# Optimization experiments

Measured on AMD Instinct MI355X. Metric: run time of the kernel, lower is better.

## Reference

```python
import jax, jax.numpy as jnp
from jax import lax
import numpy as np


def tridiagonal_solve(K, f):
    """Batched Thomas-algorithm solve of A(K) u = f.

    K: [..., m] diffusion coefficient at m grid points.
    f: broadcastable to [..., m-1] right-hand side.
    Returns u: [..., m-1].
    """
    n = K.shape[-1] - 1  # number of unknowns
    h2 = 1.0 / (n * n)
    f = jnp.broadcast_to(f, (*K.shape[:-1], n))

    denom0 = 2.0 * K[..., 0] + K[..., 1]
    c0 = -K[..., 1] / denom0  # [...]
    u0 = f[..., 0] / denom0

    # Forward elimination sweep, j = 1 .. n-2, as a scan over the grid axis.
    Kj = jnp.moveaxis(K[..., 1:n - 1], -1, 0)   # [n-2, ...] = K[..., j]
    Kj1 = jnp.moveaxis(K[..., 2:n], -1, 0)      # [n-2, ...] = K[..., j+1]
    fj = jnp.moveaxis(f[..., 1:n - 1], -1, 0)   # [n-2, ...]

    def fwd_step(carry, x):
        c_prev, u_prev = carry
        kj, kj1, fv = x
        denom = kj + kj1 + kj * c_prev
        c = -kj1 / denom
        u = (fv + kj * u_prev) / denom
        return (c, u), (c, u)

    _, (cs, us) = lax.scan(fwd_step, (c0, u0), (Kj, Kj1, fj))
    c_all = jnp.concatenate([c0[None], cs], axis=0)  # [n-1, ...] indices 0..n-2
    u_all = jnp.concatenate([u0[None], us], axis=0)  # [n-1, ...]

    Kn1 = K[..., n - 1]
    u_last = (f[..., n - 1] + Kn1 * u_all[-1]) / (Kn1 + Kn1 * c_all[-1])  # u[n-1]

    # Back substitution: u[j] -= c[j] * u[j+1], j = n-2 .. 0 (reverse scan).
    def bwd_step(u_next, x):
        cj, uj = x
        u_new = uj - cj * u_next
        return u_new, u_new

    _, u_head = lax.scan(bwd_step, u_last, (c_all, u_all), reverse=True)  # [n-1, ...]
    u_full = jnp.concatenate([u_head, u_last[None]], axis=0)  # [n, ...]
    return h2 * jnp.moveaxis(u_full, 0, -1)


def setup_inputs() -> dict:
    key = jax.random.key(0)
    k1, k2 = jax.random.split(key)
    B, M = 16384, 1024  # batch, grid points (n = M - 1 unknowns)
    alpha = jax.random.normal(k1, (B, M), dtype=jnp.float32)
    f_rhs = jax.random.normal(k2, (M - 1,), dtype=jnp.float32)
    return {"alpha": alpha, "f_rhs": f_rhs}


def reference(alpha, f_rhs):
    # DiffusionModel1d.forward: u = A(exp(alpha))^{-1} f_rhs
    return tridiagonal_solve(jnp.exp(alpha), f_rhs)
```

## Files before the change

### kernel.cpp

```cpp
#include <hip/hip_runtime.h>
#include <math.h>


constexpr int BT   = 16384;
constexpr int MPTS = 1024;
constexpr int NU   = 1023;
constexpr int CS   = 16;
constexpr int WPB  = 8;

__device__ __forceinline__ float frcp(float x) {
    float r = __builtin_amdgcn_rcpf(x);
    r = fmaf(r, fmaf(-x, r, 1.0f), r);
    return r;
}
__device__ __forceinline__ double drcp(double x) {
    double r = __builtin_amdgcn_rcp(x);
    r = fma(r, fma(-x, r, 1.0), r);
    return r;
}
__device__ __forceinline__ int sw(int j) { return j + (j >> 5); }

__global__ __launch_bounds__(WPB * 64, 6)
void pt_kernel(const float* __restrict__ alpha,
               const float* __restrict__ f_rhs,
               float* __restrict__ out) {
    const int t    = threadIdx.x;
    const int lane = t & 63;
    const int w    = t >> 6;
    const int row  = blockIdx.x * WPB + w;
    const int s    = lane * CS;

    __shared__ float f_lds[1056];
    __shared__ float ostage[WPB][1056];

    const float h2 = (float)(1.0 / (1023.0 * 1023.0));
    for (int i = t; i < NU; i += WPB * 64) f_lds[sw(i)] = h2 * f_rhs[i];
    if (t == 0) f_lds[sw(1023)] = 0.0f;

    const float* arow = alpha + (size_t)row * MPTS;
    float kf[CS + 1];
    #pragma unroll
    for (int q = 0; q < 4; ++q) {
        const float4 v = *reinterpret_cast<const float4*>(arow + s + 4 * q);
        kf[4 * q + 0] = expf(v.x);
        kf[4 * q + 1] = expf(v.y);
        kf[4 * q + 2] = expf(v.z);
        kf[4 * q + 3] = expf(v.w);
    }
    {
        float kx = (lane < 63) ? arow[s + CS] : 0.0f;
        kf[CS] = expf(kx);
    }
    if (lane == 63) kf[15] = 0.0f;

    __syncthreads();

    float cA[CS], uA[CS], vA[CS];
    {
        float cp = (lane == 0) ? 1.0f : 0.0f;
        float up = 0.0f, vp = 1.0f;
        #pragma unroll
        for (int i = 0; i < CS; ++i) {
            const int j = s + i;
            const float kc = kf[i];
            const float kn = kf[i + 1];
            const float b  = kc + kn;
            const float f  = f_lds[sw(j)];
            const float den = fmaf(kc, cp, b);
            const float r   = frcp(den);
            float ci = -kn * r;
            const float ui = fmaf(kc, up, f) * r;
            const float vi = (kc * vp) * r;
            if (i == CS - 1) ci = (lane == 63) ? 0.0f : ci;
            cA[i] = ci; uA[i] = ui; vA[i] = vi;
            cp = ci; up = ui; vp = vi;
        }
    }

    float De_f, Ae_f, Be_f, Ds_f, As_f, Bs_f;
    {
        float Dn = uA[CS - 1], An = vA[CS - 1], Bn = -cA[CS - 1];
        De_f = Dn; Ae_f = An; Be_f = Bn;
        uA[CS - 1] = Dn; vA[CS - 1] = An; cA[CS - 1] = Bn;
        #pragma unroll
        for (int i = CS - 2; i >= 0; --i) {
            const float ci = cA[i];
            Dn = fmaf(-ci, Dn, uA[i]);
            An = fmaf(-ci, An, vA[i]);
            Bn = -ci * Bn;
            uA[i] = Dn; vA[i] = An; cA[i] = Bn;
        }
        Ds_f = uA[0]; As_f = vA[0]; Bs_f = cA[0];
    }

    const double Ds = (double)Ds_f, As = (double)As_f, Bs = (double)Bs_f;
    const double De = (double)De_f, Ae = (double)Ae_f, Be = (double)Be_f;
    double m00 = Bs;
    double m01 = fma(Bs, De, -(Ds * Be));
    double m02 = Ds;
    double m11 = fma(Bs, Ae, -(As * Be));
    double m12 = As;
    double m21 = -Be;

    #pragma unroll
    for (int dlt = 1; dlt < 64; dlt <<= 1) {
        const bool val = (lane + dlt) < 64;
        double b00 = __shfl_down(m00, dlt); b00 = val ? b00 : 1.0;
        double b01 = __shfl_down(m01, dlt); b01 = val ? b01 : 0.0;
        double b02 = __shfl_down(m02, dlt); b02 = val ? b02 : 0.0;
        double b11 = __shfl_down(m11, dlt); b11 = val ? b11 : 1.0;
        double b12 = __shfl_down(m12, dlt); b12 = val ? b12 : 0.0;
        double b21 = __shfl_down(m21, dlt); b21 = val ? b21 : 0.0;
        const double n00 = m00 * b00;
        const double n01 = fma(m00, b01, fma(m01, b11, m02 * b21));
        const double n02 = fma(m00, b02, fma(m01, b12, m02));
        const double n11 = fma(m11, b11, m12 * b21);
        const double n12 = fma(m11, b12, m12);
        const double n21 = fma(m21, b11, b21);
        const double n22 = fma(m21, b12, 1.0);
        const double rn = drcp(n22);
        m00 = n00 * rn; m01 = n01 * rn; m02 = n02 * rn;
        m11 = n11 * rn; m12 = n12 * rn; m21 = n21 * rn;
    }
    const double alf = m02;
    const double bet = m12;
    double alfn = __shfl_down(alf, 1); alfn = (lane == 63) ? 0.0 : alfn;
    double betn = __shfl_down(bet, 1); betn = (lane == 63) ? 0.0 : betn;

    const double tt = drcp(fma(-Be, betn, 1.0));
    const double dl = fma(Be, alfn, De) * tt;
    const double gm = Ae * tt;

    double X = dl, G = gm;
    #pragma unroll
    for (int dlt = 1; dlt < 64; dlt <<= 1) {
        double bx = __shfl_up(X, dlt);
        double bg = __shfl_up(G, dlt);
        const bool val = lane >= dlt;
        bx = val ? bx : 0.0;
        bg = val ? bg : 1.0;
        X = fma(G, bx, X);
        G = G * bg;
    }
    double xp = __shfl_up(X, 1);
    const double uLd = (lane == 0) ? 0.0 : xp;
    const double Y   = fma(bet, uLd, alf);
    double yn = __shfl_down(Y, 1);
    const double uRd = (lane == 63) ? 0.0 : yn;

    const float uL = (float)uLd;
    const float uR = (float)uRd;
    float* ost = ostage[w];
    #pragma unroll
    for (int i = 0; i < CS; ++i) {
        const float uu = fmaf(vA[i], uL, fmaf(cA[i], uR, uA[i]));
        ost[sw(s + i)] = uu;
    }
    asm volatile("s_waitcnt lgkmcnt(0)" ::: "memory");

    float* orow = out + (size_t)row * NU;
    #pragma unroll
    for (int it = 0; it < 16; ++it) {
        const int c = it * 64 + lane;
        if (c < NU) orow[c] = ost[sw(c)];
    }
}

extern "C" void kernel_launch(void* const* d_in, const int* in_sizes, int n_in,
                              void* d_out, int out_size, void* d_ws, size_t ws_size,
                              hipStream_t stream) {
    const float* alpha = (const float*)d_in[0];
    const float* f_rhs = (const float*)d_in[1];
    float* out = (float*)d_out;

    dim3 grid(BT / WPB), block(WPB * 64);
    pt_kernel<<<grid, block, 0, stream>>>(alpha, f_rhs, out);
}
```

Measured before the change: 40.29 us.

## Replace per-chunk Thomas sweeps with division-free determinant recurrences

The local 16-element chunk solve no longer runs a Thomas forward sweep with a reciprocal per element plus a backward sweep kept in three register arrays. It uses continuant (determinant) three-term recurrences run forward and backward at the same time, with one reciprocal at the end. The final per-element solution is recomputed after the boundary values are known, from forward and reverse recurrences. This removes 16 serial reciprocals and the cA/uA/vA arrays, cutting register pressure, at the cost of recomputing the recurrences and extra FMAs. Unnormalized determinants over 16 steps can lose range or precision in fp32.

```diff
diff --git a/kernel.cpp b/kernel.cpp
--- a/kernel.cpp
+++ b/kernel.cpp
@@ -55,43 +55,45 @@
 
     __syncthreads();
 
-    float cA[CS], uA[CS], vA[CS];
-    {
-        float cp = (lane == 0) ? 1.0f : 0.0f;
-        float up = 0.0f, vp = 1.0f;
-        #pragma unroll
-        for (int i = 0; i < CS; ++i) {
-            const int j = s + i;
-            const float kc = kf[i];
-            const float kn = kf[i + 1];
-            const float b  = kc + kn;
-            const float f  = f_lds[sw(j)];
-            const float den = fmaf(kc, cp, b);
-            const float r   = frcp(den);
-            float ci = -kn * r;
-            const float ui = fmaf(kc, up, f) * r;
-            const float vi = (kc * vp) * r;
-            if (i == CS - 1) ci = (lane == 63) ? 0.0f : ci;
-            cA[i] = ci; uA[i] = ui; vA[i] = vi;
-            cp = ci; up = ui; vp = vi;
-        }
-    }
-
-    float De_f, Ae_f, Be_f, Ds_f, As_f, Bs_f;
-    {
-        float Dn = uA[CS - 1], An = vA[CS - 1], Bn = -cA[CS - 1];
-        De_f = Dn; Ae_f = An; Be_f = Bn;
-        uA[CS - 1] = Dn; vA[CS - 1] = An; cA[CS - 1] = Bn;
-        #pragma unroll
-        for (int i = CS - 2; i >= 0; --i) {
-            const float ci = cA[i];
-            Dn = fmaf(-ci, Dn, uA[i]);
-            An = fmaf(-ci, An, vA[i]);
-            Bn = -ci * Bn;
-            uA[i] = Dn; vA[i] = An; cA[i] = Bn;
-        }
-        Ds_f = uA[0]; As_f = vA[0]; Bs_f = cA[0];
-    }
+    const float a0v = (lane == 0) ? 0.0f : kf[0];
+    float dl2 = 0.0f, dl1 = 1.0f, ph1 = 0.0f, ps1 = 1.0f;
+    float rd2 = 0.0f, rd1 = 1.0f, rph = 0.0f, rps = 1.0f;
+    float d14 = 1.0f, rd1s = 1.0f;
+    #pragma unroll
+    for (int i = 0; i < CS; ++i) {
+        {
+            float b = kf[i] + kf[i + 1];
+            if (i == 0) b = (lane == 0) ? (b + kf[0]) : b;
+            const float tq = kf[i] * kf[i];
+            const float f  = f_lds[sw(s + i)];
+            const float dn = fmaf(b, dl1, -(tq * dl2));
+            const float pn = fmaf(kf[i], ph1, f * dl1);
+            const float sn = kf[i] * ps1;
+            if (i == CS - 1) d14 = dl1;
+            dl2 = dl1; dl1 = dn; ph1 = pn; ps1 = sn;
+        }
+        {
+            const int ir = CS - 1 - i;
+            float b = kf[ir] + kf[ir + 1];
+            if (ir == 0) b = (lane == 0) ? (b + kf[0]) : b;
+            const float tq = kf[ir + 1] * kf[ir + 1];
+            const float f  = f_lds[sw(s + ir)];
+            const float dn = fmaf(b, rd1, -(tq * rd2));
+            const float pn = fmaf(kf[ir + 1], rph, f * rd1);
+            const float sn = kf[ir + 1] * rps;
+            if (ir == 1) rd1s = dn;
+            rd2 = rd1; rd1 = dn; rph = pn; rps = sn;
+        }
+    }
+    const float rf = frcp(dl1);
+    const float De_f = ph1 * rf;
+    const float Ae_f = ps1 * rf;
+    float Be_f = (kf[CS] * d14) * rf;
+    Be_f = (lane == 63) ? 0.0f : Be_f;
+    const float rr = frcp(rd1);
+    const float Ds_f = rph * rr;
+    const float Bs_f = rps * rr;
+    const float As_f = (a0v * rd1s) * rr;
 
     const double Ds = (double)Ds_f, As = (double)As_f, Bs = (double)Bs_f;
     const double De = (double)De_f, Ae = (double)Ae_f, Be = (double)Be_f;
@@ -150,14 +152,42 @@
 
     const float uL = (float)uLd;
     const float uR = (float)uRd;
+    float dL[CS], sL[CS];
+    {
+        float d2 = 0.0f, d1 = 1.0f, sg = uL;
+        #pragma unroll
+        for (int i = 0; i < CS; ++i) {
+            float b = kf[i] + kf[i + 1];
+            if (i == 0) b = (lane == 0) ? (b + kf[0]) : b;
+            const float tq = kf[i] * kf[i];
+            const float f  = f_lds[sw(s + i)];
+            dL[i] = d1;
+            const float dn = fmaf(b, d1, -(tq * d2));
+            const float sn = fmaf(kf[i], sg, f * d1);
+            sL[i] = sn;
+            d2 = d1; d1 = dn; sg = sn;
+        }
+        const float invD = frcp(d1);
+        float rdd2 = 0.0f, rdd1 = 1.0f, sr = uR;
+        float* ost = ostage[w];
+        #pragma unroll
+        for (int i = 0; i < CS; ++i) {
+            const int ir = CS - 1 - i;
+            const float p  = kf[ir + 1] * sr;
+            const float uu = fmaf(rdd1, sL[ir], dL[ir] * p) * invD;
+            ost[sw(s + ir)] = uu;
+            float b = kf[ir] + kf[ir + 1];
+            if (ir == 0) b = (lane == 0) ? (b + kf[0]) : b;
+            const float tq = kf[ir + 1] * kf[ir + 1];
+            const float f  = f_lds[sw(s + ir)];
+            const float dn = fmaf(b, rdd1, -(tq * rdd2));
+            sr = fmaf(kf[ir + 1], sr, f * rdd1);
+            rdd2 = rdd1; rdd1 = dn;
+        }
+    }
+    asm volatile("s_waitcnt lgkmcnt(0)" ::: "memory");
+
     float* ost = ostage[w];
-    #pragma unroll
-    for (int i = 0; i < CS; ++i) {
-        const float uu = fmaf(vA[i], uL, fmaf(cA[i], uR, uA[i]));
-        ost[sw(s + i)] = uu;
-    }
-    asm volatile("s_waitcnt lgkmcnt(0)" ::: "memory");
-
     float* orow = out + (size_t)row * NU;
     #pragma unroll
     for (int it = 0; it < 16; ++it) {
```

Measured after the change: 95.10 us. 2.36x slower.
